# Performance work log

Measured on AMD Instinct MI355X. Metric: run time of the kernel, lower is better.

Reference implementation:

```python
import jax, jax.numpy as jnp
import numpy as np

N, E = 50000, 800000
F_IN, F_EMB1, F_EMB2, F_HID, F_OUT = 128, 512, 128, 1024, 64


def _linear_params(k, fan_in, fan_out):
    s = 1.0 / np.sqrt(fan_in)
    kw, kb = jax.random.split(k)
    W = jax.random.uniform(kw, (fan_in, fan_out), jnp.float32, -s, s)
    b = jax.random.uniform(kb, (fan_out,), jnp.float32, -s, s)
    return W, b


def setup_inputs() -> dict:
    key = jax.random.key(0)
    ks = jax.random.split(key, 8)
    x = jax.random.normal(ks[0], (N, F_IN), jnp.float32)
    src = jax.random.randint(ks[1], (E,), 0, N)
    dst = jax.random.randint(ks[2], (E,), 0, N)
    edge_index = jnp.stack([src, dst])  # [2, E]
    edge_weight = jax.random.uniform(ks[3], (E,), jnp.float32)  # positive weights
    W1, b1 = _linear_params(ks[4], F_IN, F_EMB1)
    W2, b2 = _linear_params(ks[5], F_EMB1, F_EMB2)
    W3, b3 = _linear_params(ks[6], F_EMB2, F_HID)
    W4, b4 = _linear_params(ks[7], F_HID, F_OUT)
    return dict(x=x, edge_index=edge_index, edge_weight=edge_weight,
                W1=W1, b1=b1, W2=W2, b2=b2, W3=W3, b3=b3, W4=W4, b4=b4)


def gcn_conv(x, src, dst, w, W, b):
    """PyG GCNConv: transform, then sym-normalized weighted aggregation with self-loops.
    out = D^{-1/2} (A_w + I) D^{-1/2} (x W) + b,  deg = scatter(w @ dst) + 1."""
    n = x.shape[0]
    h = x @ W  # [N, F_out]
    deg = jax.ops.segment_sum(w, dst, num_segments=n) + 1.0  # +1 for self-loop weight
    dinv = jax.lax.rsqrt(deg)
    norm = dinv[src] * w * dinv[dst]  # [E]
    agg = jax.ops.segment_sum(norm[:, None] * h[src], dst, num_segments=n)
    agg = agg + h / deg[:, None]  # self-loop: dinv[i]*1*dinv[i] * h[i]
    return agg + b


def reference(x, edge_index, edge_weight, W1, b1, W2, b2, W3, b3, W4, b4):
    src, dst = edge_index[0], edge_index[1]
    h = jax.nn.relu(gcn_conv(x, src, dst, edge_weight, W1, b1))
    # graph_normalization=False -> identity; dropout is identity in eval mode
    h = jax.nn.relu(gcn_conv(h, src, dst, edge_weight, W2, b2))
    h = jax.nn.relu(h @ W3 + b3)
    out = jax.nn.relu(h @ W4 + b4)
    return out
```

## Files before the change

### kernel.cpp

```cpp
#include <hip/hip_runtime.h>


#define ELLW 64
#define C64S 16

typedef short bf16x8 __attribute__((ext_vector_type(8)));
typedef float f32x4 __attribute__((ext_vector_type(4)));

__device__ __forceinline__ unsigned short f2b(float f) {
    unsigned u = __builtin_bit_cast(unsigned, f);
    unsigned r = (u + 0x7FFFu + ((u >> 16) & 1u)) >> 16;
    return (unsigned short)r;
}
__device__ __forceinline__ float b2f(unsigned short u) {
    return __builtin_bit_cast(float, (unsigned)u << 16);
}

__global__ void k_setup(const float* __restrict__ x,
                        const float* __restrict__ W1, const float* __restrict__ W2,
                        const float* __restrict__ W3, const float* __restrict__ W4,
                        unsigned short* __restrict__ W1t, unsigned short* __restrict__ W2t,
                        unsigned short* __restrict__ W3t, unsigned short* __restrict__ W4t,
                        unsigned short* __restrict__ xb,
                        const int* __restrict__ src, const int* __restrict__ dst,
                        const float* __restrict__ ew,
                        unsigned long long* __restrict__ cnt64,
                        int2* __restrict__ s_edge, int Nn, int E) {
    int b = blockIdx.x;
    if (b < 3125) {
        int e = b * 256 + threadIdx.x;
        if (e < E) {
            int d = dst[e];
            float wv = ew[e];
            unsigned wfix = (unsigned)(wv * 8388608.0f);
            unsigned long long add = ((unsigned long long)1 << 32) | wfix;
            unsigned long long old = atomicAdd(&cnt64[(size_t)d * C64S], add);
            int slot = (int)(old >> 32);
            if (slot < ELLW)
                s_edge[(size_t)d * ELLW + slot] =
                    make_int2(src[e], __builtin_bit_cast(int, wv));
        }
    } else if (b < 4405) {
        int i = (b - 3125) * 256 + threadIdx.x;
        if (i < 65536) {
            int k = i >> 9, n = i & 511;
            W1t[n * 128 + k] = f2b(W1[i]);
        } else if (i < 131072) {
            int j = i - 65536; int k = j >> 7, n = j & 127;
            W2t[n * 512 + k] = f2b(W2[j]);
        } else if (i < 262144) {
            int j = i - 131072; int k = j >> 10, n = j & 1023;
            W3t[n * 128 + k] = f2b(W3[j]);
        } else {
            int j = i - 262144; int k = j >> 6, n = j & 63;
            W4t[n * 1024 + k] = f2b(W4[j]);
        }
    } else {
        int i = (b - 4405) * 256 + threadIdx.x;
        if (i < Nn * 32) {
            float4 v = ((const float4*)x)[i];
            ushort4 o;
            o.x = f2b(v.x); o.y = f2b(v.y); o.z = f2b(v.z); o.w = f2b(v.w);
            ((ushort4*)xb)[i] = o;
        }
    }
}

__global__ void k_deg(const unsigned long long* __restrict__ cnt64,
                      float* __restrict__ dinv, int Nn) {
    int i = blockIdx.x * 256 + threadIdx.x;
    if (i >= Nn) return;
    unsigned long long cv = cnt64[(size_t)i * C64S];
    float deg = 1.0f + (float)(unsigned)(cv & 0xFFFFFFFFull) * (1.0f / 8388608.0f);
    dinv[i] = rsqrtf(deg);
}

template <bool FIRST, bool BIAS_RELU>
__global__ __launch_bounds__(256) void k_gather(
    const unsigned short* __restrict__ Xb, int2* __restrict__ s_edge,
    const unsigned long long* __restrict__ cnt64, const float* __restrict__ dinv,
    const float* __restrict__ bias, unsigned short* __restrict__ outb, int Nn) {
    int node = blockIdx.x * 4 + (threadIdx.x >> 6);
    if (node >= Nn) return;
    int lane = threadIdx.x & 63;
    float di = dinv[node];
    float dii = di * di;
    ushort2 sv = ((const ushort2*)(Xb + (size_t)node * 128))[lane];
    float ax = b2f(sv.x) * dii, ay = b2f(sv.y) * dii;

    int c = min((int)(cnt64[(size_t)node * C64S] >> 32), ELLW);
    size_t base = (size_t)node * ELLW;
    int sreg = 0;
    float nv = 0.0f;
    if (lane < c) {
        int2 rec = s_edge[base + lane];
        sreg = rec.x;
        if (FIRST) {
            float wv = __builtin_bit_cast(float, rec.y);
            nv = dinv[sreg] * wv * di;
            ((int*)s_edge)[2 * (base + lane) + 1] = __builtin_bit_cast(int, nv);
        } else {
            nv = __builtin_bit_cast(float, rec.y);
        }
    }

    int j = 0;
    for (; j + 8 <= c; j += 8) {
        int s0 = __shfl(sreg, j),     s1 = __shfl(sreg, j + 1);
        int s2 = __shfl(sreg, j + 2), s3 = __shfl(sreg, j + 3);
        int s4 = __shfl(sreg, j + 4), s5 = __shfl(sreg, j + 5);
        int s6 = __shfl(sreg, j + 6), s7 = __shfl(sreg, j + 7);
        float n0 = __shfl(nv, j),     n1 = __shfl(nv, j + 1);
        float n2 = __shfl(nv, j + 2), n3 = __shfl(nv, j + 3);
        float n4 = __shfl(nv, j + 4), n5 = __shfl(nv, j + 5);
        float n6 = __shfl(nv, j + 6), n7 = __shfl(nv, j + 7);
        ushort2 r0 = ((const ushort2*)(Xb + (size_t)s0 * 128))[lane];
        ushort2 r1 = ((const ushort2*)(Xb + (size_t)s1 * 128))[lane];
        ushort2 r2 = ((const ushort2*)(Xb + (size_t)s2 * 128))[lane];
        ushort2 r3 = ((const ushort2*)(Xb + (size_t)s3 * 128))[lane];
        ushort2 r4 = ((const ushort2*)(Xb + (size_t)s4 * 128))[lane];
        ushort2 r5 = ((const ushort2*)(Xb + (size_t)s5 * 128))[lane];
        ushort2 r6 = ((const ushort2*)(Xb + (size_t)s6 * 128))[lane];
        ushort2 r7 = ((const ushort2*)(Xb + (size_t)s7 * 128))[lane];
        ax += n0 * b2f(r0.x) + n1 * b2f(r1.x) + n2 * b2f(r2.x) + n3 * b2f(r3.x);
        ay += n0 * b2f(r0.y) + n1 * b2f(r1.y) + n2 * b2f(r2.y) + n3 * b2f(r3.y);
        ax += n4 * b2f(r4.x) + n5 * b2f(r5.x) + n6 * b2f(r6.x) + n7 * b2f(r7.x);
        ay += n4 * b2f(r4.y) + n5 * b2f(r5.y) + n6 * b2f(r6.y) + n7 * b2f(r7.y);
    }
    for (; j < c; ++j) {
        int sj = __shfl(sreg, j);
        float nj = __shfl(nv, j);
        ushort2 r = ((const ushort2*)(Xb + (size_t)sj * 128))[lane];
        ax += nj * b2f(r.x);
        ay += nj * b2f(r.y);
    }

    if (BIAS_RELU) {
        float2 bv = ((const float2*)bias)[lane];
        ax = fmaxf(ax + bv.x, 0.0f);
        ay = fmaxf(ay + bv.y, 0.0f);
    }
    ushort2 o; o.x = f2b(ax); o.y = f2b(ay);
    ((ushort2*)(outb + (size_t)node * 128))[lane] = o;
}

template <int H, int OUTW, bool HAS_BO, bool OUT_BF16>
__global__ __launch_bounds__(256) void k_mlp(
    const unsigned short* __restrict__ A, const unsigned short* __restrict__ Wht,
    const unsigned short* __restrict__ Wot, const float* __restrict__ bh,
    const float* __restrict__ bo, void* __restrict__ out, int M) {
    constexpr int HC = H / 64;
    constexpr int NJ = OUTW / 16;
    constexpr int OW4 = OUTW / 32;
    __shared__ __align__(16) unsigned short Whs[64 * 128];
    __shared__ __align__(16) unsigned short Ps[128 * 64];
    __shared__ __align__(16) unsigned short Wos[OUTW * 64];
    const int tid = threadIdx.x, wave = tid >> 6, lane = tid & 63;
    const int lm = lane & 15, quad = lane >> 4;
    const int bm0 = blockIdx.x * 128;

    bf16x8 af[2][4];
    #pragma unroll
    for (int i = 0; i < 2; ++i) {
        int gr = bm0 + wave * 32 + i * 16 + lm;
        #pragma unroll
        for (int kb = 0; kb < 4; ++kb) af[i][kb] = bf16x8{0, 0, 0, 0, 0, 0, 0, 0};
        if (gr < M) {
            #pragma unroll
            for (int kb = 0; kb < 4; ++kb)
                af[i][kb] = *(const bf16x8*)(A + (size_t)gr * 128 + kb * 32 + quad * 8);
        }
    }

    #pragma unroll
    for (int u = 0; u < 4; ++u) {
        int idx = tid + u * 256; int r = idx >> 4, g = idx & 15;
        *(int4*)&Whs[r * 128 + ((g ^ (r & 15)) * 8)] =
            *(const int4*)(Wht + (size_t)r * 128 + g * 8);
    }
    #pragma unroll
    for (int u = 0; u < OW4; ++u) {
        int idx = tid + u * 256; int r = idx >> 3, g = idx & 7;
        *(int4*)&Wos[r * 64 + ((g ^ (r & 7)) * 8)] =
            *(const int4*)(Wot + (size_t)r * H + g * 8);
    }
    __syncthreads();

    f32x4 oacc[2][NJ] = {};
    for (int c = 0; c < HC; ++c) {
        f32x4 hacc[2][4] = {};
        #pragma unroll
        for (int kb = 0; kb < 4; ++kb) {
            bf16x8 bfr[4];
            #pragma unroll
            for (int j = 0; j < 4; ++j) {
                int r = j * 16 + lm, g = kb * 4 + quad;
                bfr[j] = *(const bf16x8*)&Whs[r * 128 + ((g ^ (r & 15)) * 8)];
            }
            #pragma unroll
            for (int i = 0; i < 2; ++i)
                #pragma unroll
                for (int j = 0; j < 4; ++j)
                    hacc[i][j] = __builtin_amdgcn_mfma_f32_16x16x32_bf16(
                        af[i][kb], bfr[j], hacc[i][j], 0, 0, 0);
        }

        #pragma unroll
        for (int i = 0; i < 2; ++i) {
            #pragma unroll
            for (int j = 0; j < 4; ++j) {
                int col = j * 16 + lm;
                float bv = bh[c * 64 + col];
                #pragma unroll
                for (int r4 = 0; r4 < 4; ++r4) {
                    int row = wave * 32 + i * 16 + quad * 4 + r4;
                    float o = fmaxf(hacc[i][j][r4] + bv, 0.0f);
                    Ps[row * 64 + (((col >> 3) ^ (row & 7)) * 8) + (col & 7)] = f2b(o);
                }
            }
        }

        #pragma unroll
        for (int kb = 0; kb < 2; ++kb) {
            bf16x8 pf[2];
            #pragma unroll
            for (int i = 0; i < 2; ++i) {
                int r = wave * 32 + i * 16 + lm, g = kb * 4 + quad;
                pf[i] = *(const bf16x8*)&Ps[r * 64 + ((g ^ (r & 7)) * 8)];
            }
            #pragma unroll
            for (int j = 0; j < NJ; ++j) {
                int r = j * 16 + lm, g = kb * 4 + quad;
                bf16x8 wf = *(const bf16x8*)&Wos[r * 64 + ((g ^ (r & 7)) * 8)];
                #pragma unroll
                for (int i = 0; i < 2; ++i)
                    oacc[i][j] = __builtin_amdgcn_mfma_f32_16x16x32_bf16(
                        pf[i], wf, oacc[i][j], 0, 0, 0);
            }
        }

        if (c + 1 < HC) {
            __syncthreads();
            #pragma unroll
            for (int u = 0; u < 4; ++u) {
                int idx = tid + u * 256; int r = idx >> 4, g = idx & 15;
                *(int4*)&Whs[r * 128 + ((g ^ (r & 15)) * 8)] =
                    *(const int4*)(Wht + (size_t)((c + 1) * 64 + r) * 128 + g * 8);
            }
            #pragma unroll
            for (int u = 0; u < OW4; ++u) {
                int idx = tid + u * 256; int r = idx >> 3, g = idx & 7;
                *(int4*)&Wos[r * 64 + ((g ^ (r & 7)) * 8)] =
                    *(const int4*)(Wot + (size_t)r * H + (c + 1) * 64 + g * 8);
            }
            __syncthreads();
        }
    }

    #pragma unroll
    for (int i = 0; i < 2; ++i) {
        #pragma unroll
        for (int j = 0; j < NJ; ++j) {
            int col = j * 16 + lm;
            float bv = HAS_BO ? bo[col] : 0.0f;
            #pragma unroll
            for (int r4 = 0; r4 < 4; ++r4) {
                int m = bm0 + wave * 32 + i * 16 + quad * 4 + r4;
                if (m < M) {
                    float o = oacc[i][j][r4];
                    if (HAS_BO) o = fmaxf(o + bv, 0.0f);
                    if (OUT_BF16)
                        ((unsigned short*)out)[(size_t)m * OUTW + col] = f2b(o);
                    else
                        ((float*)out)[(size_t)m * OUTW + col] = o;
                }
            }
        }
    }
}

static inline int cdiv(long a, long b) { return (int)((a + b - 1) / b); }

extern "C" void kernel_launch(void* const* d_in, const int* in_sizes, int n_in,
                              void* d_out, int out_size, void* d_ws, size_t ws_size,
                              hipStream_t stream) {
    const float* x  = (const float*)d_in[0];
    const int*   ei = (const int*)d_in[1];
    const float* ew = (const float*)d_in[2];
    const float* W1 = (const float*)d_in[3];
    const float* b1 = (const float*)d_in[4];
    const float* W2 = (const float*)d_in[5];
    const float* b2 = (const float*)d_in[6];
    const float* W3 = (const float*)d_in[7];
    const float* b3 = (const float*)d_in[8];
    const float* W4 = (const float*)d_in[9];
    const float* b4 = (const float*)d_in[10];
    const int Nn = in_sizes[0] / 128;
    const int E  = in_sizes[1] / 2;
    const int* src = ei;
    const int* dst = ei + E;

    char* ws = (char*)d_ws;
    size_t off_b = 0;
    auto alloc = [&](size_t bytes) -> void* {
        void* p = ws + off_b;
        off_b += (bytes + 255) & ~(size_t)255;
        return p;
    };
    float*              dinv   = (float*)alloc((size_t)Nn * 4);
    unsigned long long* cnt64  = (unsigned long long*)alloc((size_t)Nn * C64S * 8);
    int2*               s_edge = (int2*)alloc((size_t)Nn * ELLW * 8);
    unsigned short*     W1t    = (unsigned short*)alloc(512 * 128 * 2);
    unsigned short*     W2t    = (unsigned short*)alloc(128 * 512 * 2);
    unsigned short*     W3t    = (unsigned short*)alloc(1024 * 128 * 2);
    unsigned short*     W4t    = (unsigned short*)alloc(64 * 1024 * 2);
    unsigned short*     xb     = (unsigned short*)alloc((size_t)Nn * 128 * 2);
    unsigned short*     t2b    = (unsigned short*)alloc((size_t)Nn * 128 * 2);
    unsigned short*     actb   = (unsigned short*)alloc((size_t)Nn * 128 * 2);
    float*              out    = (float*)d_out;

    hipMemsetAsync(cnt64, 0, (size_t)Nn * C64S * 8, stream);
    k_setup<<<10655, 256, 0, stream>>>(x, W1, W2, W3, W4, W1t, W2t, W3t, W4t,
                                       xb, src, dst, ew, cnt64, s_edge, Nn, E);
    k_deg<<<cdiv(Nn, 256), 256, 0, stream>>>(cnt64, dinv, Nn);

    k_gather<true, false><<<cdiv(Nn, 4), 256, 0, stream>>>(
        xb, s_edge, cnt64, dinv, nullptr, actb, Nn);
    k_mlp<512, 128, false, true><<<cdiv(Nn, 128), 256, 0, stream>>>(
        actb, W1t, W2t, b1, nullptr, t2b, Nn);

    k_gather<false, true><<<cdiv(Nn, 4), 256, 0, stream>>>(
        t2b, s_edge, cnt64, dinv, b2, actb, Nn);

    k_mlp<1024, 64, true, false><<<cdiv(Nn, 128), 256, 0, stream>>>(
        actb, W3t, W4t, b3, b4, out, Nn);
}
```

Measured before the change: 285.1 us.

## Fuse gather and MLP stages into a persistent work-queue kernel with tile flags

Each gather kernel and the MLP kernel that follows it are merged into one persistent kernel of 784 blocks. Blocks pull tasks from atomic counters, running all 128-node gather tiles first and then MLP tiles. Each MLP tile waits on a per-tile done flag that is published with release/acquire atomics. The aim is to let the MLP work overlap the tail of the gather and to cut kernel launch boundaries. In exchange, fewer waves are in flight for the latency-bound gather, since each wave now processes 32 nodes one after another, and the shared-memory footprint of the MLP path lowers occupancy during the gather phase.

```diff
diff --git a/kernel.cpp b/kernel.cpp
--- a/kernel.cpp
+++ b/kernel.cpp
@@ -75,204 +75,241 @@
     dinv[i] = rsqrtf(deg);
 }
 
-template <bool FIRST, bool BIAS_RELU>
-__global__ __launch_bounds__(256) void k_gather(
+template <bool FIRST, bool BIAS_RELU, int H, int OUTW, bool HAS_BO, bool OUT_BF16>
+__global__ __launch_bounds__(256) void k_pair(
     const unsigned short* __restrict__ Xb, int2* __restrict__ s_edge,
     const unsigned long long* __restrict__ cnt64, const float* __restrict__ dinv,
-    const float* __restrict__ bias, unsigned short* __restrict__ outb, int Nn) {
-    int node = blockIdx.x * 4 + (threadIdx.x >> 6);
-    if (node >= Nn) return;
-    int lane = threadIdx.x & 63;
-    float di = dinv[node];
-    float dii = di * di;
-    ushort2 sv = ((const ushort2*)(Xb + (size_t)node * 128))[lane];
-    float ax = b2f(sv.x) * dii, ay = b2f(sv.y) * dii;
-
-    int c = min((int)(cnt64[(size_t)node * C64S] >> 32), ELLW);
-    size_t base = (size_t)node * ELLW;
-    int sreg = 0;
-    float nv = 0.0f;
-    if (lane < c) {
-        int2 rec = s_edge[base + lane];
-        sreg = rec.x;
-        if (FIRST) {
-            float wv = __builtin_bit_cast(float, rec.y);
-            nv = dinv[sreg] * wv * di;
-            ((int*)s_edge)[2 * (base + lane) + 1] = __builtin_bit_cast(int, nv);
-        } else {
-            nv = __builtin_bit_cast(float, rec.y);
-        }
-    }
-
-    int j = 0;
-    for (; j + 8 <= c; j += 8) {
-        int s0 = __shfl(sreg, j),     s1 = __shfl(sreg, j + 1);
-        int s2 = __shfl(sreg, j + 2), s3 = __shfl(sreg, j + 3);
-        int s4 = __shfl(sreg, j + 4), s5 = __shfl(sreg, j + 5);
-        int s6 = __shfl(sreg, j + 6), s7 = __shfl(sreg, j + 7);
-        float n0 = __shfl(nv, j),     n1 = __shfl(nv, j + 1);
-        float n2 = __shfl(nv, j + 2), n3 = __shfl(nv, j + 3);
-        float n4 = __shfl(nv, j + 4), n5 = __shfl(nv, j + 5);
-        float n6 = __shfl(nv, j + 6), n7 = __shfl(nv, j + 7);
-        ushort2 r0 = ((const ushort2*)(Xb + (size_t)s0 * 128))[lane];
-        ushort2 r1 = ((const ushort2*)(Xb + (size_t)s1 * 128))[lane];
-        ushort2 r2 = ((const ushort2*)(Xb + (size_t)s2 * 128))[lane];
-        ushort2 r3 = ((const ushort2*)(Xb + (size_t)s3 * 128))[lane];
-        ushort2 r4 = ((const ushort2*)(Xb + (size_t)s4 * 128))[lane];
-        ushort2 r5 = ((const ushort2*)(Xb + (size_t)s5 * 128))[lane];
-        ushort2 r6 = ((const ushort2*)(Xb + (size_t)s6 * 128))[lane];
-        ushort2 r7 = ((const ushort2*)(Xb + (size_t)s7 * 128))[lane];
-        ax += n0 * b2f(r0.x) + n1 * b2f(r1.x) + n2 * b2f(r2.x) + n3 * b2f(r3.x);
-        ay += n0 * b2f(r0.y) + n1 * b2f(r1.y) + n2 * b2f(r2.y) + n3 * b2f(r3.y);
-        ax += n4 * b2f(r4.x) + n5 * b2f(r5.x) + n6 * b2f(r6.x) + n7 * b2f(r7.x);
-        ay += n4 * b2f(r4.y) + n5 * b2f(r5.y) + n6 * b2f(r6.y) + n7 * b2f(r7.y);
-    }
-    for (; j < c; ++j) {
-        int sj = __shfl(sreg, j);
-        float nj = __shfl(nv, j);
-        ushort2 r = ((const ushort2*)(Xb + (size_t)sj * 128))[lane];
-        ax += nj * b2f(r.x);
-        ay += nj * b2f(r.y);
-    }
-
-    if (BIAS_RELU) {
-        float2 bv = ((const float2*)bias)[lane];
-        ax = fmaxf(ax + bv.x, 0.0f);
-        ay = fmaxf(ay + bv.y, 0.0f);
-    }
-    ushort2 o; o.x = f2b(ax); o.y = f2b(ay);
-    ((ushort2*)(outb + (size_t)node * 128))[lane] = o;
-}
-
-template <int H, int OUTW, bool HAS_BO, bool OUT_BF16>
-__global__ __launch_bounds__(256) void k_mlp(
-    const unsigned short* __restrict__ A, const unsigned short* __restrict__ Wht,
-    const unsigned short* __restrict__ Wot, const float* __restrict__ bh,
-    const float* __restrict__ bo, void* __restrict__ out, int M) {
+    const float* __restrict__ gbias, unsigned short* __restrict__ gout,
+    const unsigned short* __restrict__ Wht, const unsigned short* __restrict__ Wot,
+    const float* __restrict__ bh, const float* __restrict__ bo,
+    void* __restrict__ out, int Nn, int* __restrict__ qctl) {
     constexpr int HC = H / 64;
     constexpr int NJ = OUTW / 16;
     constexpr int OW4 = OUTW / 32;
     __shared__ __align__(16) unsigned short Whs[64 * 128];
     __shared__ __align__(16) unsigned short Ps[128 * 64];
     __shared__ __align__(16) unsigned short Wos[OUTW * 64];
+    __shared__ int s_task;
     const int tid = threadIdx.x, wave = tid >> 6, lane = tid & 63;
     const int lm = lane & 15, quad = lane >> 4;
-    const int bm0 = blockIdx.x * 128;
-
-    bf16x8 af[2][4];
-    #pragma unroll
-    for (int i = 0; i < 2; ++i) {
-        int gr = bm0 + wave * 32 + i * 16 + lm;
-        #pragma unroll
-        for (int kb = 0; kb < 4; ++kb) af[i][kb] = bf16x8{0, 0, 0, 0, 0, 0, 0, 0};
-        if (gr < M) {
-            #pragma unroll
-            for (int kb = 0; kb < 4; ++kb)
-                af[i][kb] = *(const bf16x8*)(A + (size_t)gr * 128 + kb * 32 + quad * 8);
-        }
-    }
-
-    #pragma unroll
-    for (int u = 0; u < 4; ++u) {
-        int idx = tid + u * 256; int r = idx >> 4, g = idx & 15;
-        *(int4*)&Whs[r * 128 + ((g ^ (r & 15)) * 8)] =
-            *(const int4*)(Wht + (size_t)r * 128 + g * 8);
-    }
-    #pragma unroll
-    for (int u = 0; u < OW4; ++u) {
-        int idx = tid + u * 256; int r = idx >> 3, g = idx & 7;
-        *(int4*)&Wos[r * 64 + ((g ^ (r & 7)) * 8)] =
-            *(const int4*)(Wot + (size_t)r * H + g * 8);
-    }
-    __syncthreads();
-
-    f32x4 oacc[2][NJ] = {};
-    for (int c = 0; c < HC; ++c) {
-        f32x4 hacc[2][4] = {};
-        #pragma unroll
-        for (int kb = 0; kb < 4; ++kb) {
-            bf16x8 bfr[4];
-            #pragma unroll
-            for (int j = 0; j < 4; ++j) {
-                int r = j * 16 + lm, g = kb * 4 + quad;
-                bfr[j] = *(const bf16x8*)&Whs[r * 128 + ((g ^ (r & 15)) * 8)];
-            }
-            #pragma unroll
-            for (int i = 0; i < 2; ++i)
-                #pragma unroll
-                for (int j = 0; j < 4; ++j)
-                    hacc[i][j] = __builtin_amdgcn_mfma_f32_16x16x32_bf16(
-                        af[i][kb], bfr[j], hacc[i][j], 0, 0, 0);
-        }
-
-        #pragma unroll
-        for (int i = 0; i < 2; ++i) {
-            #pragma unroll
-            for (int j = 0; j < 4; ++j) {
-                int col = j * 16 + lm;
-                float bv = bh[c * 64 + col];
-                #pragma unroll
-                for (int r4 = 0; r4 < 4; ++r4) {
-                    int row = wave * 32 + i * 16 + quad * 4 + r4;
-                    float o = fmaxf(hacc[i][j][r4] + bv, 0.0f);
-                    Ps[row * 64 + (((col >> 3) ^ (row & 7)) * 8) + (col & 7)] = f2b(o);
-                }
-            }
-        }
-
-        #pragma unroll
-        for (int kb = 0; kb < 2; ++kb) {
-            bf16x8 pf[2];
+    const int NT = (Nn + 127) >> 7;
+    int* g_next = qctl;
+    int* m_next = qctl + 1;
+    int* done   = qctl + 2;
+
+    while (true) {
+        __syncthreads();
+        if (tid == 0) {
+            int g = atomicAdd(g_next, 1);
+            if (g < NT) s_task = g;
+            else {
+                int m = atomicAdd(m_next, 1);
+                s_task = (m < NT) ? (0x40000000 | m) : -1;
+            }
+        }
+        __syncthreads();
+        int task = s_task;
+        if (task < 0) return;
+
+        if (!(task & 0x40000000)) {
+            int g = task;
+            for (int n = 0; n < 32; ++n) {
+                int node = g * 128 + wave * 32 + n;
+                if (node >= Nn) break;
+                float di = dinv[node];
+                float dii = di * di;
+                ushort2 sv = ((const ushort2*)(Xb + (size_t)node * 128))[lane];
+                float ax = b2f(sv.x) * dii, ay = b2f(sv.y) * dii;
+
+                int c = min((int)(cnt64[(size_t)node * C64S] >> 32), ELLW);
+                size_t base = (size_t)node * ELLW;
+                int sreg = 0;
+                float nv = 0.0f;
+                if (lane < c) {
+                    int2 rec = s_edge[base + lane];
+                    sreg = rec.x;
+                    if (FIRST) {
+                        float wv = __builtin_bit_cast(float, rec.y);
+                        nv = dinv[sreg] * wv * di;
+                        ((int*)s_edge)[2 * (base + lane) + 1] =
+                            __builtin_bit_cast(int, nv);
+                    } else {
+                        nv = __builtin_bit_cast(float, rec.y);
+                    }
+                }
+
+                int j = 0;
+                for (; j + 8 <= c; j += 8) {
+                    int s0 = __shfl(sreg, j),     s1 = __shfl(sreg, j + 1);
+                    int s2 = __shfl(sreg, j + 2), s3 = __shfl(sreg, j + 3);
+                    int s4 = __shfl(sreg, j + 4), s5 = __shfl(sreg, j + 5);
+                    int s6 = __shfl(sreg, j + 6), s7 = __shfl(sreg, j + 7);
+                    float n0 = __shfl(nv, j),     n1 = __shfl(nv, j + 1);
+                    float n2 = __shfl(nv, j + 2), n3 = __shfl(nv, j + 3);
+                    float n4 = __shfl(nv, j + 4), n5 = __shfl(nv, j + 5);
+                    float n6 = __shfl(nv, j + 6), n7 = __shfl(nv, j + 7);
+                    ushort2 r0 = ((const ushort2*)(Xb + (size_t)s0 * 128))[lane];
+                    ushort2 r1 = ((const ushort2*)(Xb + (size_t)s1 * 128))[lane];
+                    ushort2 r2 = ((const ushort2*)(Xb + (size_t)s2 * 128))[lane];
+                    ushort2 r3 = ((const ushort2*)(Xb + (size_t)s3 * 128))[lane];
+                    ushort2 r4 = ((const ushort2*)(Xb + (size_t)s4 * 128))[lane];
+                    ushort2 r5 = ((const ushort2*)(Xb + (size_t)s5 * 128))[lane];
+                    ushort2 r6 = ((const ushort2*)(Xb + (size_t)s6 * 128))[lane];
+                    ushort2 r7 = ((const ushort2*)(Xb + (size_t)s7 * 128))[lane];
+                    ax += n0 * b2f(r0.x) + n1 * b2f(r1.x) + n2 * b2f(r2.x) + n3 * b2f(r3.x);
+                    ay += n0 * b2f(r0.y) + n1 * b2f(r1.y) + n2 * b2f(r2.y) + n3 * b2f(r3.y);
+                    ax += n4 * b2f(r4.x) + n5 * b2f(r5.x) + n6 * b2f(r6.x) + n7 * b2f(r7.x);
+                    ay += n4 * b2f(r4.y) + n5 * b2f(r5.y) + n6 * b2f(r6.y) + n7 * b2f(r7.y);
+                }
+                for (; j < c; ++j) {
+                    int sj = __shfl(sreg, j);
+                    float nj = __shfl(nv, j);
+                    ushort2 r = ((const ushort2*)(Xb + (size_t)sj * 128))[lane];
+                    ax += nj * b2f(r.x);
+                    ay += nj * b2f(r.y);
+                }
+
+                if (BIAS_RELU) {
+                    float2 bv = ((const float2*)gbias)[lane];
+                    ax = fmaxf(ax + bv.x, 0.0f);
+                    ay = fmaxf(ay + bv.y, 0.0f);
+                }
+                ushort2 o; o.x = f2b(ax); o.y = f2b(ay);
+                ((ushort2*)(gout + (size_t)node * 128))[lane] = o;
+            }
+            __threadfence();
+            __syncthreads();
+            if (tid == 0)
+                __hip_atomic_store(&done[g], 1, __ATOMIC_RELEASE,
+                                   __HIP_MEMORY_SCOPE_AGENT);
+        } else {
+            int m = task & 0x3FFFFFFF;
+            if (tid == 0) {
+                while (__hip_atomic_load(&done[m], __ATOMIC_ACQUIRE,
+                                         __HIP_MEMORY_SCOPE_AGENT) == 0)
+                    __builtin_amdgcn_s_sleep(16);
+            }
+            __syncthreads();
+            __threadfence();
+
+            const int bm0 = m * 128;
+            bf16x8 af[2][4];
             #pragma unroll
             for (int i = 0; i < 2; ++i) {
-                int r = wave * 32 + i * 16 + lm, g = kb * 4 + quad;
-                pf[i] = *(const bf16x8*)&Ps[r * 64 + ((g ^ (r & 7)) * 8)];
-            }
-            #pragma unroll
-            for (int j = 0; j < NJ; ++j) {
-                int r = j * 16 + lm, g = kb * 4 + quad;
-                bf16x8 wf = *(const bf16x8*)&Wos[r * 64 + ((g ^ (r & 7)) * 8)];
-                #pragma unroll
-                for (int i = 0; i < 2; ++i)
-                    oacc[i][j] = __builtin_amdgcn_mfma_f32_16x16x32_bf16(
-                        pf[i], wf, oacc[i][j], 0, 0, 0);
-            }
-        }
-
-        if (c + 1 < HC) {
-            __syncthreads();
+                int gr = bm0 + wave * 32 + i * 16 + lm;
+                #pragma unroll
+                for (int kb = 0; kb < 4; ++kb) af[i][kb] = bf16x8{0,0,0,0,0,0,0,0};
+                if (gr < Nn) {
+                    #pragma unroll
+                    for (int kb = 0; kb < 4; ++kb)
+                        af[i][kb] = *(const bf16x8*)(gout + (size_t)gr * 128 +
+                                                     kb * 32 + quad * 8);
+                }
+            }
+
             #pragma unroll
             for (int u = 0; u < 4; ++u) {
-                int idx = tid + u * 256; int r = idx >> 4, g = idx & 15;
-                *(int4*)&Whs[r * 128 + ((g ^ (r & 15)) * 8)] =
-                    *(const int4*)(Wht + (size_t)((c + 1) * 64 + r) * 128 + g * 8);
+                int idx = tid + u * 256; int r = idx >> 4, gg = idx & 15;
+                *(int4*)&Whs[r * 128 + ((gg ^ (r & 15)) * 8)] =
+                    *(const int4*)(Wht + (size_t)r * 128 + gg * 8);
             }
             #pragma unroll
             for (int u = 0; u < OW4; ++u) {
-                int idx = tid + u * 256; int r = idx >> 3, g = idx & 7;
-                *(int4*)&Wos[r * 64 + ((g ^ (r & 7)) * 8)] =
-                    *(const int4*)(Wot + (size_t)r * H + (c + 1) * 64 + g * 8);
+                int idx = tid + u * 256; int r = idx >> 3, gg = idx & 7;
+                *(int4*)&Wos[r * 64 + ((gg ^ (r & 7)) * 8)] =
+                    *(const int4*)(Wot + (size_t)r * H + gg * 8);
             }
             __syncthreads();
-        }
-    }
-
-    #pragma unroll
-    for (int i = 0; i < 2; ++i) {
-        #pragma unroll
-        for (int j = 0; j < NJ; ++j) {
-            int col = j * 16 + lm;
-            float bv = HAS_BO ? bo[col] : 0.0f;
+
+            f32x4 oacc[2][NJ] = {};
+            for (int c = 0; c < HC; ++c) {
+                f32x4 hacc[2][4] = {};
+                #pragma unroll
+                for (int kb = 0; kb < 4; ++kb) {
+                    bf16x8 bfr[4];
+                    #pragma unroll
+                    for (int j = 0; j < 4; ++j) {
+                        int r = j * 16 + lm, gg = kb * 4 + quad;
+                        bfr[j] = *(const bf16x8*)&Whs[r * 128 + ((gg ^ (r & 15)) * 8)];
+                    }
+                    #pragma unroll
+                    for (int i = 0; i < 2; ++i)
+                        #pragma unroll
+                        for (int j = 0; j < 4; ++j)
+                            hacc[i][j] = __builtin_amdgcn_mfma_f32_16x16x32_bf16(
+                                af[i][kb], bfr[j], hacc[i][j], 0, 0, 0);
+                }
+
+                #pragma unroll
+                for (int i = 0; i < 2; ++i) {
+                    #pragma unroll
+                    for (int j = 0; j < 4; ++j) {
+                        int col = j * 16 + lm;
+                        float bv = bh[c * 64 + col];
+                        #pragma unroll
+                        for (int r4 = 0; r4 < 4; ++r4) {
+                            int row = wave * 32 + i * 16 + quad * 4 + r4;
+                            float o = fmaxf(hacc[i][j][r4] + bv, 0.0f);
+                            Ps[row * 64 + (((col >> 3) ^ (row & 7)) * 8) + (col & 7)] = f2b(o);
+                        }
+                    }
+                }
+
+                #pragma unroll
+                for (int kb = 0; kb < 2; ++kb) {
+                    bf16x8 pf[2];
+                    #pragma unroll
+                    for (int i = 0; i < 2; ++i) {
+                        int r = wave * 32 + i * 16 + lm, gg = kb * 4 + quad;
+                        pf[i] = *(const bf16x8*)&Ps[r * 64 + ((gg ^ (r & 7)) * 8)];
+                    }
+                    #pragma unroll
+                    for (int j = 0; j < NJ; ++j) {
+                        int r = j * 16 + lm, gg = kb * 4 + quad;
+                        bf16x8 wf = *(const bf16x8*)&Wos[r * 64 + ((gg ^ (r & 7)) * 8)];
+                        #pragma unroll
+                        for (int i = 0; i < 2; ++i)
+                            oacc[i][j] = __builtin_amdgcn_mfma_f32_16x16x32_bf16(
+                                pf[i], wf, oacc[i][j], 0, 0, 0);
+                    }
+                }
+
+                if (c + 1 < HC) {
+                    __syncthreads();
+                    #pragma unroll
+                    for (int u = 0; u < 4; ++u) {
+                        int idx = tid + u * 256; int r = idx >> 4, gg = idx & 15;
+                        *(int4*)&Whs[r * 128 + ((gg ^ (r & 15)) * 8)] =
+                            *(const int4*)(Wht + (size_t)((c + 1) * 64 + r) * 128 + gg * 8);
+                    }
+                    #pragma unroll
+                    for (int u = 0; u < OW4; ++u) {
+                        int idx = tid + u * 256; int r = idx >> 3, gg = idx & 7;
+                        *(int4*)&Wos[r * 64 + ((gg ^ (r & 7)) * 8)] =
+                            *(const int4*)(Wot + (size_t)r * H + (c + 1) * 64 + gg * 8);
+                    }
+                    __syncthreads();
+                }
+            }
+
             #pragma unroll
-            for (int r4 = 0; r4 < 4; ++r4) {
-                int m = bm0 + wave * 32 + i * 16 + quad * 4 + r4;
-                if (m < M) {
-                    float o = oacc[i][j][r4];
-                    if (HAS_BO) o = fmaxf(o + bv, 0.0f);
-                    if (OUT_BF16)
-                        ((unsigned short*)out)[(size_t)m * OUTW + col] = f2b(o);
-                    else
-                        ((float*)out)[(size_t)m * OUTW + col] = o;
+            for (int i = 0; i < 2; ++i) {
+                #pragma unroll
+                for (int j = 0; j < NJ; ++j) {
+                    int col = j * 16 + lm;
+                    float bv = HAS_BO ? bo[col] : 0.0f;
+                    #pragma unroll
+                    for (int r4 = 0; r4 < 4; ++r4) {
+                        int mm = bm0 + wave * 32 + i * 16 + quad * 4 + r4;
+                        if (mm < Nn) {
+                            float o = oacc[i][j][r4];
+                            if (HAS_BO) o = fmaxf(o + bv, 0.0f);
+                            if (OUT_BF16)
+                                ((unsigned short*)out)[(size_t)mm * OUTW + col] = f2b(o);
+                            else
+                                ((float*)out)[(size_t)mm * OUTW + col] = o;
+                        }
+                    }
                 }
             }
         }
@@ -309,6 +346,7 @@
     };
     float*              dinv   = (float*)alloc((size_t)Nn * 4);
     unsigned long long* cnt64  = (unsigned long long*)alloc((size_t)Nn * C64S * 8);
+    int*                qctl   = (int*)alloc(1024 * 4);
     int2*               s_edge = (int2*)alloc((size_t)Nn * ELLW * 8);
     unsigned short*     W1t    = (unsigned short*)alloc(512 * 128 * 2);
     unsigned short*     W2t    = (unsigned short*)alloc(128 * 512 * 2);
@@ -319,19 +357,16 @@
     unsigned short*     actb   = (unsigned short*)alloc((size_t)Nn * 128 * 2);
     float*              out    = (float*)d_out;
 
-    hipMemsetAsync(cnt64, 0, (size_t)Nn * C64S * 8, stream);
+    hipMemsetAsync(cnt64, 0, (size_t)Nn * C64S * 8 + 1024 * 4, stream);
     k_setup<<<10655, 256, 0, stream>>>(x, W1, W2, W3, W4, W1t, W2t, W3t, W4t,
                                        xb, src, dst, ew, cnt64, s_edge, Nn, E);
     k_deg<<<cdiv(Nn, 256), 256, 0, stream>>>(cnt64, dinv, Nn);
 
-    k_gather<true, false><<<cdiv(Nn, 4), 256, 0, stream>>>(
-        xb, s_edge, cnt64, dinv, nullptr, actb, Nn);
-    k_mlp<512, 128, false, true><<<cdiv(Nn, 128), 256, 0, stream>>>(
-        actb, W1t, W2t, b1, nullptr, t2b, Nn);
-
-    k_gather<false, true><<<cdiv(Nn, 4), 256, 0, stream>>>(
-        t2b, s_edge, cnt64, dinv, b2, actb, Nn);
-
-    k_mlp<1024, 64, true, false><<<cdiv(Nn, 128), 256, 0, stream>>>(
-        actb, W3t, W4t, b3, b4, out, Nn);
-}
+    k_pair<true, false, 512, 128, false, true><<<784, 256, 0, stream>>>(
+        xb, s_edge, cnt64, dinv, nullptr, actb, W1t, W2t, b1, nullptr,
+        t2b, Nn, qctl);
+
+    k_pair<false, true, 1024, 64, true, false><<<784, 256, 0, stream>>>(
+        t2b, s_edge, cnt64, dinv, b2, actb, W3t, W4t, b3, b4,
+        out, Nn, qctl + 512);
+}
```

Result: slower. 842.3 us (+195.4%).
